# Kernel tuning notes

Measured on AMD Instinct MI355X. Metric: run time of the kernel, lower is better.

## Reference

```python
import jax, jax.numpy as jnp
import numpy as np

T, B, E, H, L = 512, 64, 300, 800, 3  # seq, batch, embed, per-layer hidden, layers


def setup_inputs() -> dict:
    key = jax.random.key(0)
    ks = jax.random.split(key, 8)
    s = 0.05
    return {
        "sent": jax.random.normal(ks[0], (T, B, E), jnp.float32),
        "lengths": jax.random.randint(ks[1], (B,), 1, T + 1),
        "W0": jax.random.normal(ks[2], (E, 3 * H), jnp.float32) * s,
        "b0": jnp.zeros((3 * H,), jnp.float32),
        "W1": jax.random.normal(ks[3], (H, 3 * H), jnp.float32) * s,
        "b1": jnp.zeros((3 * H,), jnp.float32),
        "W2": jax.random.normal(ks[4], (H, 3 * H), jnp.float32) * s,
        "b2": jnp.zeros((3 * H,), jnp.float32),
    }


def _fo_pool(f, z):
    # c_t = f_t * z_t + (1 - f_t) * c_{t-1}, c_0 = 0  (ForgetMult)
    # linear recurrence c_t = a_t * c_{t-1} + b_t with a = 1-f, b = f*z
    a = 1.0 - f
    b = f * z
    def comb(c1, c2):
        a1, b1 = c1
        a2, b2 = c2
        return (a2 * a1, a2 * b1 + b2)
    _, C = jax.lax.associative_scan(comb, (a, b), axis=0)
    return C  # [T,B,H]; initial state is zero so C is exactly the pooled state


def _qrnn_layer(x, W, b):
    g = jnp.einsum('tbe,eh->tbh', x, W) + b  # [T,B,3H]
    z, f, o = jnp.split(g, 3, axis=-1)
    C = _fo_pool(jax.nn.sigmoid(f), jnp.tanh(z))
    return jax.nn.sigmoid(o) * C, C[-1]


def reference(sent, lengths, W0, b0, W1, b1, W2, b2):
    h = sent
    finals = []
    for W, bb in ((W0, b0), (W1, b1), (W2, b2)):
        h, c_last = _qrnn_layer(h, W, bb)
        finals.append(c_last)
    hn = jnp.stack(finals, axis=0)            # [L,B,H]
    out = jnp.transpose(hn, (1, 0, 2)).reshape(B, L * H)  # [B, L*H]
    return out
```

## Files before the change

### kernel.cpp

```cpp
#include <hip/hip_runtime.h>
#include <hip/hip_bf16.h>
#include <cstdint>
#include <cstddef>


typedef __bf16 bf16_t;
typedef __bf16 bf16x8 __attribute__((ext_vector_type(8)));
typedef float f32x4 __attribute__((ext_vector_type(4)));

#define T_C 128
#define NCHUNK 4
#define BATCH 64
#define EMB 300
#define HID 800
#define LDH 832
#define MC (T_C * BATCH)
#define CAST_OPS (MC * 320 / 8)

__device__ __forceinline__ float fast_sigmoid(float x) {
  return 1.0f / (1.0f + __expf(-x));
}
__device__ __forceinline__ float fast_tanh(float x) {
  return 2.0f / (1.0f + __expf(-2.0f * x)) - 1.0f;
}
__device__ __forceinline__ float b2f(uint32_t u) {
  union { uint32_t i; float f; } x;
  x.i = u << 16;
  return x.f;
}

__device__ __forceinline__ void cast_op(const float* __restrict__ X,
                                        bf16_t* __restrict__ Y, int cc,
                                        int id) {
  const int rr = id / 40, cb = id - rr * 40;
  const int b = rr >> 7, t = rr & 127;
  const float* src = X + (size_t)((cc * 128 + t) * 64 + b) * EMB + cb * 8;
  bf16x8 w;
  if (cb < 37) {
    const f32x4 v0 = *(const f32x4*)src;
    const f32x4 v1 = *(const f32x4*)(src + 4);
#pragma unroll
    for (int e = 0; e < 4; ++e) {
      w[e] = (bf16_t)v0[e];
      w[e + 4] = (bf16_t)v1[e];
    }
  } else {
#pragma unroll
    for (int e = 0; e < 8; ++e) {
      const int col = cb * 8 + e;
      float v = (col < EMB) ? src[e] : (col == EMB ? 1.0f : 0.0f);
      w[e] = (bf16_t)v;
    }
  }
  *(bf16x8*)&Y[((size_t)cc * MC + rr) * 320 + cb * 8] = w;
}

__global__ __launch_bounds__(256) void prep_all(
    const float* __restrict__ W0, const float* __restrict__ W1,
    const float* __restrict__ W2, const float* __restrict__ B0,
    const float* __restrict__ B1, const float* __restrict__ B2,
    bf16_t* __restrict__ M0, bf16_t* __restrict__ M1, bf16_t* __restrict__ Z2,
    const float* __restrict__ sent, bf16_t* __restrict__ A0) {
  const int z = blockIdx.z;
  if (z == 3) {
    const int id = (blockIdx.y * gridDim.x + blockIdx.x) * 256 + threadIdx.x;
    if (id < CAST_OPS) cast_op(sent, A0, 0, id);
    return;
  }
  const float* W = z == 0 ? W0 : (z == 1 ? W1 : W2);
  const float* Bv = z == 0 ? B0 : (z == 1 ? B1 : B2);
  bf16_t* Wt = z == 0 ? M0 : (z == 1 ? M1 : Z2);
  const int K = z == 0 ? 300 : 800;
  const int Kpad = z == 0 ? 320 : 832;
  const int Npad = (z < 2) ? 2496 : 1664;
  const int i = blockIdx.x, j = blockIdx.y;
  if (i * 32 >= Npad || j * 32 >= Kpad) return;
  __shared__ float tile[32][33];
  const int tx = threadIdx.x & 31, ty = threadIdx.x >> 5;
#pragma unroll
  for (int r = 0; r < 32; r += 8) {
    const int k = j * 32 + ty + r;
    const int n = i * 32 + tx;
    int h, src;
    if (z < 2) {
      const int jt = n / 192, rr = n - jt * 192;
      if (rr < 128) {
        h = jt * 64 + (rr >> 1);
        src = (rr & 1) * 800 + h;
      } else {
        h = jt * 64 + (rr - 128);
        src = 1600 + h;
      }
    } else {
      h = n >> 1;
      src = (n & 1) * 800 + h;
    }
    float v = 0.0f;
    if (h < 800) {
      if (k < K) v = W[(size_t)k * 2400 + src];
      else if (k == K) v = Bv[src];
    }
    tile[ty + r][tx] = v;
  }
  __syncthreads();
#pragma unroll
  for (int r = 0; r < 32; r += 8) {
    const int n = i * 32 + ty + r, k = j * 32 + tx;
    if (n < Npad && k < Kpad)
      Wt[(size_t)n * Kpad + k] = (bf16_t)tile[tx][ty + r];
  }
}

__device__ __forceinline__ void stage16(const bf16_t* gp, bf16_t* lp) {
  __builtin_amdgcn_global_load_lds((__attribute__((address_space(1))) void*)gp,
                                   (__attribute__((address_space(3))) void*)lp,
                                   16, 0, 0);
}

template <int NTF, int ETS>
__device__ __forceinline__ void gemm_tile_to_lds(
    const bf16_t* __restrict__ A, const bf16_t* __restrict__ Bt,
    bf16_t* __restrict__ S, int K, int mBase, int nBase) {
  bf16_t* As = S;
  bf16_t* Bs = S + 8192;
  const int tid = threadIdx.x;
  const int wave = tid >> 6, lane = tid & 63;
  const int wm = wave >> 1, wn = wave & 1;
  const int srow = tid >> 3;
  const int scolSw = ((tid & 7) ^ (srow & 7)) * 8;
  const size_t aBase = (size_t)(mBase + srow) * K + scolSw;
  const size_t bBase = (size_t)(nBase + srow) * K + scolSw;
  const int ldsOff = tid * 8;

  f32x4 acc[4][NTF];
#pragma unroll
  for (int mt = 0; mt < 4; ++mt)
#pragma unroll
    for (int nt = 0; nt < NTF; ++nt) {
      f32x4 zz = {0.0f, 0.0f, 0.0f, 0.0f};
      acc[mt][nt] = zz;
    }

  const int fr = lane & 15, fq = lane >> 4;
  const int x0 = fr & 7;
  const int ckEl0 = (fq ^ x0) * 8;
  const int ckEl1 = ((4 + fq) ^ x0) * 8;

  for (int k0 = 0; k0 < K; k0 += 64) {
#pragma unroll
    for (int p = 0; p < 4; ++p)
      stage16(A + aBase + (size_t)(32 * p) * K + k0, &As[ldsOff + p * 2048]);
#pragma unroll
    for (int p = 0; p < NTF; ++p)
      stage16(Bt + bBase + (size_t)(32 * p) * K + k0, &Bs[ldsOff + p * 2048]);
    __syncthreads();
#pragma unroll
    for (int kh = 0; kh < 2; ++kh) {
      const int ck = kh ? ckEl1 : ckEl0;
      bf16x8 af[4], bfv[NTF];
#pragma unroll
      for (int mt = 0; mt < 4; ++mt)
        af[mt] = *(const bf16x8*)&As[(wm * 64 + mt * 16 + fr) * 64 + ck];
#pragma unroll
      for (int nt = 0; nt < NTF; ++nt)
        bfv[nt] = *(const bf16x8*)&Bs[(wn * (16 * NTF) + nt * 16 + fr) * 64 + ck];
#pragma unroll
      for (int mt = 0; mt < 4; ++mt)
#pragma unroll
        for (int nt = 0; nt < NTF; ++nt)
          acc[mt][nt] = __builtin_amdgcn_mfma_f32_16x16x32_bf16(
              af[mt], bfv[nt], acc[mt][nt], 0, 0, 0);
    }
    __syncthreads();
  }
  bf16_t* Et = S;
#pragma unroll
  for (int mt = 0; mt < 4; ++mt)
#pragma unroll
    for (int nt = 0; nt < NTF; ++nt)
#pragma unroll
      for (int r = 0; r < 4; ++r)
        Et[(wm * 64 + mt * 16 + fq * 4 + r) * ETS + wn * (16 * NTF) + nt * 16 +
           fr] = (bf16_t)acc[mt][nt][r];
  __syncthreads();
}

__device__ __forceinline__ void scan_h_body(
    const bf16_t* __restrict__ A, const bf16_t* __restrict__ Wm,
    bf16_t* __restrict__ Hout, float* __restrict__ carry,
    float* __restrict__ outC, int K, int outOff, int first, int last, int b,
    int ntile, bf16_t* S, float (*SA)[64], float (*SB)[64], float (*SC)[64]) {
  gemm_tile_to_lds<6, 196>(A, Wm, S, K, b * 128, ntile * 192);

  const uint32_t* Ep = (const uint32_t*)S;
  const int tid = threadIdx.x;
  const int hl = tid & 63, s = tid >> 6;
  const int h = ntile * 64 + hl;
  const bool hOK = (h < HID);

  float av[32], bv[32];
  float Aa = 1.0f, Bb = 0.0f;
#pragma unroll
  for (int q = 0; q < 32; ++q) {
    const int t = s * 32 + q;
    const uint32_t v = Ep[t * 98 + hl];
    const float zv = fast_tanh(b2f(v & 0xffffu));
    const float fv = fast_sigmoid(b2f(v >> 16));
    av[q] = 1.0f - fv;
    bv[q] = fv * zv;
    Aa *= av[q];
    Bb = fmaf(av[q], Bb, bv[q]);
  }
  SA[s][hl] = Aa;
  SB[s][hl] = Bb;
  __syncthreads();
  if (tid < 64) {
    const int h2 = ntile * 64 + tid;
    const bool ok2 = (h2 < HID);
    float c = (first || !ok2) ? 0.0f : carry[b * HID + h2];
#pragma unroll
    for (int ss = 0; ss < 4; ++ss) {
      SC[ss][tid] = c;
      c = fmaf(SA[ss][tid], c, SB[ss][tid]);
    }
    if (ok2) {
      carry[b * HID + h2] = c;
      if (last) outC[b * 2400 + outOff + h2] = c;
    }
  }
  __syncthreads();
  const bf16_t padv = (h == HID) ? (bf16_t)1.0f : (bf16_t)0.0f;
  float c = SC[s][hl];
#pragma unroll
  for (int q = 0; q < 32; ++q) {
    const int t = s * 32 + q;
    c = fmaf(av[q], c, bv[q]);
    const float o = fast_sigmoid((float)S[t * 196 + 128 + hl]);
    Hout[(size_t)(b * 128 + t) * LDH + h] = hOK ? (bf16_t)(o * c) : padv;
  }
}

__device__ __forceinline__ void scan_c_body(
    const bf16_t* __restrict__ A, const bf16_t* __restrict__ Wzf,
    float* __restrict__ carry, float* __restrict__ outC, int K, int outOff,
    int first, int last, int b, int ntile, bf16_t* S, float (*SA)[64],
    float (*SB)[64]) {
  gemm_tile_to_lds<4, 140>(A, Wzf, S, K, b * 128, ntile * 128);

  const uint32_t* Ep = (const uint32_t*)S;
  const int tid = threadIdx.x;
  const int hl = tid & 63, s = tid >> 6;

  float Aa = 1.0f, Bb = 0.0f;
#pragma unroll
  for (int q = 0; q < 32; ++q) {
    const int t = s * 32 + q;
    const uint32_t v = Ep[t * 70 + hl];
    const float zv = fast_tanh(b2f(v & 0xffffu));
    const float fv = fast_sigmoid(b2f(v >> 16));
    const float a = 1.0f - fv;
    Aa *= a;
    Bb = fmaf(a, Bb, fv * zv);
  }
  SA[s][hl] = Aa;
  SB[s][hl] = Bb;
  __syncthreads();
  if (tid < 64) {
    const int h2 = ntile * 64 + tid;
    const bool ok2 = (h2 < HID);
    float c = (first || !ok2) ? 0.0f : carry[b * HID + h2];
#pragma unroll
    for (int ss = 0; ss < 4; ++ss) c = fmaf(SA[ss][tid], c, SB[ss][tid]);
    if (ok2) {
      carry[b * HID + h2] = c;
      if (last) outC[b * 2400 + outOff + h2] = c;
    }
  }
}

__device__ __forceinline__ void block_tile(int& b, int& ntile) {
  const int nT = 13;
  const int L = blockIdx.y * nT + blockIdx.x;
  const int xcd = L & 7, j = L >> 3;
  b = xcd * 8 + j / nT;
  ntile = j % nT;
}

struct Role {
  const bf16_t* A;
  const bf16_t* W;
  bf16_t* Hout;
  float* carry;
  int K;
  int outOff;
  int type;
  int first;
  int last;
};

__global__ __launch_bounds__(256, 3) void gemm_scan_multi(
    Role r0, Role r1, Role r2, Role r3, float* __restrict__ outC) {
  __shared__ __align__(16) bf16_t S[25088];
  __shared__ float SA[4][64], SB[4][64], SC[4][64];
  const Role r = blockIdx.z == 0
                     ? r0
                     : (blockIdx.z == 1 ? r1 : (blockIdx.z == 2 ? r2 : r3));
  if (r.type == 3) {
    int id = (blockIdx.y * gridDim.x + blockIdx.x) * 256 + threadIdx.x;
    const int stride = gridDim.x * gridDim.y * 256;
#pragma unroll
    for (int it = 0; it < 2; ++it, id += stride)
      if (id < CAST_OPS) cast_op((const float*)r.A, r.Hout, r.outOff, id);
    return;
  }
  int b, ntile;
  block_tile(b, ntile);
  if (r.type == 1)
    scan_h_body(r.A, r.W, r.Hout, r.carry, outC, r.K, r.outOff, r.first,
                r.last, b, ntile, S, SA, SB, SC);
  else
    scan_c_body(r.A, r.W, r.carry, outC, r.K, r.outOff, r.first, r.last, b,
                ntile, S, SA, SB);
}

__global__ __launch_bounds__(256, 4) void gemm_scan_c4(
    const bf16_t* __restrict__ A, const bf16_t* __restrict__ Wzf,
    float* __restrict__ carry, float* __restrict__ outC, int K, int outOff,
    int first, int last) {
  __shared__ __align__(16) bf16_t S[17920];
  __shared__ float SA[4][64], SB[4][64];
  int b, ntile;
  block_tile(b, ntile);
  scan_c_body(A, Wzf, carry, outC, K, outOff, first, last, b, ntile, S, SA,
              SB);
}

extern "C" void kernel_launch(void* const* d_in, const int* in_sizes, int n_in,
                              void* d_out, int out_size, void* d_ws, size_t ws_size,
                              hipStream_t stream) {
  const float* sent = (const float*)d_in[0];
  const float* W0 = (const float*)d_in[2];
  const float* b0 = (const float*)d_in[3];
  const float* W1 = (const float*)d_in[4];
  const float* b1 = (const float*)d_in[5];
  const float* W2 = (const float*)d_in[6];
  const float* b2 = (const float*)d_in[7];
  float* out = (float*)d_out;

  char* ws = (char*)d_ws;
  size_t off = 0;
  auto alloc = [&](size_t bytes) {
    void* p = ws + off;
    off += (bytes + 255) & ~(size_t)255;
    return p;
  };
  bf16_t* Wm0 = (bf16_t*)alloc((size_t)2496 * 320 * 2);
  bf16_t* Wm1 = (bf16_t*)alloc((size_t)2496 * 832 * 2);
  bf16_t* Wzf2 = (bf16_t*)alloc((size_t)1664 * 832 * 2);
  bf16_t* A0 = (bf16_t*)alloc((size_t)32768 * 320 * 2);
  bf16_t* H0buf[2], *H1buf[2];
  H0buf[0] = (bf16_t*)alloc((size_t)MC * LDH * 2);
  H0buf[1] = (bf16_t*)alloc((size_t)MC * LDH * 2);
  H1buf[0] = (bf16_t*)alloc((size_t)MC * LDH * 2);
  H1buf[1] = (bf16_t*)alloc((size_t)MC * LDH * 2);
  float* car0 = (float*)alloc((size_t)BATCH * HID * 4);
  float* car1 = (float*)alloc((size_t)BATCH * HID * 4);
  float* car2 = (float*)alloc((size_t)BATCH * HID * 4);
  if (off > ws_size) return;

  prep_all<<<dim3(78, 26, 4), 256, 0, stream>>>(W0, W1, W2, b0, b1, b2, Wm0,
                                                Wm1, Wzf2, sent, A0);

  auto mkL0 = [&](int c) -> Role {
    return Role{A0 + (size_t)c * MC * 320, Wm0, H0buf[c & 1], car0,
                320, 0, 1, c == 0, c == NCHUNK - 1};
  };
  auto mkL1 = [&](int c) -> Role {
    return Role{H0buf[c & 1], Wm1, H1buf[c & 1], car1,
                832, 800, 1, c == 0, c == NCHUNK - 1};
  };
  auto mkL2 = [&](int c) -> Role {
    return Role{H1buf[c & 1], Wzf2, nullptr, car2,
                832, 1600, 2, c == 0, c == NCHUNK - 1};
  };
  auto mkCast = [&](int c) -> Role {
    return Role{(const bf16_t*)sent, nullptr, A0, nullptr, 0, c, 3, 0, 0};
  };

  {
    Role a = mkL0(0), c1 = mkCast(1), c2 = mkCast(2), c3 = mkCast(3);
    gemm_scan_multi<<<dim3(13, 64, 4), 256, 0, stream>>>(a, c1, c2, c3, out);
  }
  {
    Role a = mkL1(0), b_ = mkL0(1);
    gemm_scan_multi<<<dim3(13, 64, 2), 256, 0, stream>>>(a, b_, b_, b_, out);
  }
  for (int c = 1; c <= 2; ++c) {
    Role a = mkL1(c), b_ = mkL2(c - 1), d = mkL0(c + 1);
    gemm_scan_multi<<<dim3(13, 64, 3), 256, 0, stream>>>(a, b_, d, d, out);
  }
  {
    Role a = mkL1(3), b_ = mkL2(2);
    gemm_scan_multi<<<dim3(13, 64, 2), 256, 0, stream>>>(a, b_, b_, b_, out);
  }
  gemm_scan_c4<<<dim3(13, 64), 256, 0, stream>>>(H1buf[1], Wzf2, car2, out,
                                                 832, 1600, 0, 1);
}
```

Before: 461.7 us.

## Scan directly on MFMA accumulator registers instead of staging GEMM output in LDS

Removes the LDS epilogue that wrote the GEMM tile as bf16 and read it back for the forget-mult scan. The scan now runs on the MFMA accumulator registers directly, using 8 time segments per column. For this to work, the weight columns and the time rows of the input are permuted so that z/f/o for the same hidden unit land in matching lanes. The LDS footprint shrinks and a sync disappears, at the cost of more registers per thread and a more involved permutation of rows and weights. Explicit bf16 rounding of a and b is kept so numerics stay close to the previous path.

```diff
diff --git a/kernel.cpp b/kernel.cpp
--- a/kernel.cpp
+++ b/kernel.cpp
@@ -28,13 +28,22 @@
   x.i = u << 16;
   return x.f;
 }
+__device__ __forceinline__ uint32_t f2u16(float v) {
+  union { bf16_t h; uint16_t u; } x;
+  x.h = (bf16_t)v;
+  return (uint32_t)x.u;
+}
+
+__device__ __forceinline__ int rowperm(int i) {
+  return (i & 0xC3) | ((i & 0x30) >> 2) | ((i & 0x0C) << 2);
+}
 
 __device__ __forceinline__ void cast_op(const float* __restrict__ X,
                                         bf16_t* __restrict__ Y, int cc,
                                         int id) {
   const int rr = id / 40, cb = id - rr * 40;
-  const int b = rr >> 7, t = rr & 127;
-  const float* src = X + (size_t)((cc * 128 + t) * 64 + b) * EMB + cb * 8;
+  const int b = rr >> 7, tl = rowperm(rr & 127);
+  const float* src = X + (size_t)((cc * 128 + tl) * 64 + b) * EMB + cb * 8;
   bf16x8 w;
   if (cb < 37) {
     const f32x4 v0 = *(const f32x4*)src;
@@ -83,17 +92,23 @@
     const int n = i * 32 + tx;
     int h, src;
     if (z < 2) {
-      const int jt = n / 192, rr = n - jt * 192;
-      if (rr < 128) {
-        h = jt * 64 + (rr >> 1);
-        src = (rr & 1) * 800 + h;
+      const int jt = n / 192, u0 = n - jt * 192;
+      const int w = u0 / 96, u = u0 - w * 96;
+      if (u < 64) {
+        const int p = u >> 5, g = (u >> 4) & 1, fc = u & 15;
+        h = jt * 64 + w * 32 + p * 16 + fc;
+        src = g * 800 + h;
       } else {
-        h = jt * 64 + (rr - 128);
+        const int q = u - 64;
+        h = jt * 64 + w * 32 + q;
         src = 1600 + h;
       }
     } else {
-      h = n >> 1;
-      src = (n & 1) * 800 + h;
+      const int jt = n >> 7, u0 = n & 127;
+      const int w = u0 >> 6, u = u0 & 63;
+      const int p = u >> 5, g = (u >> 4) & 1, fc = u & 15;
+      h = jt * 64 + w * 32 + p * 16 + fc;
+      src = g * 800 + h;
     }
     float v = 0.0f;
     if (h < 800) {
@@ -117,10 +132,11 @@
                                    16, 0, 0);
 }
 
-template <int NTF, int ETS>
-__device__ __forceinline__ void gemm_tile_to_lds(
+template <int NTF>
+__device__ __forceinline__ void gemm_tile_regs(
     const bf16_t* __restrict__ A, const bf16_t* __restrict__ Bt,
-    bf16_t* __restrict__ S, int K, int mBase, int nBase) {
+    bf16_t* __restrict__ S, int K, int mBase, int nBase,
+    f32x4 (&acc)[4][NTF]) {
   bf16_t* As = S;
   bf16_t* Bs = S + 8192;
   const int tid = threadIdx.x;
@@ -132,7 +148,6 @@
   const size_t bBase = (size_t)(nBase + srow) * K + scolSw;
   const int ldsOff = tid * 8;
 
-  f32x4 acc[4][NTF];
 #pragma unroll
   for (int mt = 0; mt < 4; ++mt)
 #pragma unroll
@@ -173,16 +188,6 @@
     }
     __syncthreads();
   }
-  bf16_t* Et = S;
-#pragma unroll
-  for (int mt = 0; mt < 4; ++mt)
-#pragma unroll
-    for (int nt = 0; nt < NTF; ++nt)
-#pragma unroll
-      for (int r = 0; r < 4; ++r)
-        Et[(wm * 64 + mt * 16 + fq * 4 + r) * ETS + wn * (16 * NTF) + nt * 16 +
-           fr] = (bf16_t)acc[mt][nt][r];
-  __syncthreads();
 }
 
 __device__ __forceinline__ void scan_h_body(
@@ -190,36 +195,43 @@
     bf16_t* __restrict__ Hout, float* __restrict__ carry,
     float* __restrict__ outC, int K, int outOff, int first, int last, int b,
     int ntile, bf16_t* S, float (*SA)[64], float (*SB)[64], float (*SC)[64]) {
-  gemm_tile_to_lds<6, 196>(A, Wm, S, K, b * 128, ntile * 192);
-
-  const uint32_t* Ep = (const uint32_t*)S;
+  f32x4 acc[4][6];
+  gemm_tile_regs<6>(A, Wm, S, K, b * 128, ntile * 192, acc);
+
   const int tid = threadIdx.x;
-  const int hl = tid & 63, s = tid >> 6;
-  const int h = ntile * 64 + hl;
-  const bool hOK = (h < HID);
-
-  float av[32], bv[32];
-  float Aa = 1.0f, Bb = 0.0f;
-#pragma unroll
-  for (int q = 0; q < 32; ++q) {
-    const int t = s * 32 + q;
-    const uint32_t v = Ep[t * 98 + hl];
-    const float zv = fast_tanh(b2f(v & 0xffffu));
-    const float fv = fast_sigmoid(b2f(v >> 16));
-    av[q] = 1.0f - fv;
-    bv[q] = fv * zv;
-    Aa *= av[q];
-    Bb = fmaf(av[q], Bb, bv[q]);
-  }
-  SA[s][hl] = Aa;
-  SB[s][hl] = Bb;
+  const int wave = tid >> 6, lane = tid & 63;
+  const int wm = wave >> 1, wn = wave & 1;
+  const int fr = lane & 15, fq = lane >> 4;
+  const int seg = wm * 4 + fq;
+
+  uint32_t ab[2][16];
+#pragma unroll
+  for (int p = 0; p < 2; ++p) {
+    float Aa = 1.0f, Bb = 0.0f;
+#pragma unroll
+    for (int mt = 0; mt < 4; ++mt)
+#pragma unroll
+      for (int r = 0; r < 4; ++r) {
+        const int q = mt * 4 + r;
+        const float zv = fast_tanh(acc[mt][2 * p][r]);
+        const float fv = fast_sigmoid(acc[mt][2 * p + 1][r]);
+        const uint32_t ua = f2u16(1.0f - fv), ub = f2u16(fv * zv);
+        ab[p][q] = ua | (ub << 16);
+        const float af = b2f(ua), bf_ = b2f(ub << 16 >> 16);
+        Aa *= af;
+        Bb = fmaf(af, Bb, b2f(ub));
+      }
+    const int cl = wn * 32 + p * 16 + fr;
+    SA[seg][cl] = Aa;
+    SB[seg][cl] = Bb;
+  }
   __syncthreads();
   if (tid < 64) {
     const int h2 = ntile * 64 + tid;
     const bool ok2 = (h2 < HID);
     float c = (first || !ok2) ? 0.0f : carry[b * HID + h2];
 #pragma unroll
-    for (int ss = 0; ss < 4; ++ss) {
+    for (int ss = 0; ss < 8; ++ss) {
       SC[ss][tid] = c;
       c = fmaf(SA[ss][tid], c, SB[ss][tid]);
     }
@@ -229,14 +241,23 @@
     }
   }
   __syncthreads();
-  const bf16_t padv = (h == HID) ? (bf16_t)1.0f : (bf16_t)0.0f;
-  float c = SC[s][hl];
-#pragma unroll
-  for (int q = 0; q < 32; ++q) {
-    const int t = s * 32 + q;
-    c = fmaf(av[q], c, bv[q]);
-    const float o = fast_sigmoid((float)S[t * 196 + 128 + hl]);
-    Hout[(size_t)(b * 128 + t) * LDH + h] = hOK ? (bf16_t)(o * c) : padv;
+#pragma unroll
+  for (int p = 0; p < 2; ++p) {
+    const int cl = wn * 32 + p * 16 + fr;
+    const int h = ntile * 64 + cl;
+    const bool hOK = (h < HID);
+    const bf16_t padv = (h == HID) ? (bf16_t)1.0f : (bf16_t)0.0f;
+    float c = SC[seg][cl];
+#pragma unroll
+    for (int mt = 0; mt < 4; ++mt)
+#pragma unroll
+      for (int r = 0; r < 4; ++r) {
+        const int q = mt * 4 + r;
+        c = fmaf(b2f(ab[p][q] & 0xffffu), c, b2f(ab[p][q] >> 16));
+        const float o = fast_sigmoid(acc[mt][4 + p][r]);
+        const int row = b * 128 + wm * 64 + mt * 16 + fq * 4 + r;
+        Hout[(size_t)row * LDH + h] = hOK ? (bf16_t)(o * c) : padv;
+      }
   }
 }
 
@@ -245,32 +266,40 @@
     float* __restrict__ carry, float* __restrict__ outC, int K, int outOff,
     int first, int last, int b, int ntile, bf16_t* S, float (*SA)[64],
     float (*SB)[64]) {
-  gemm_tile_to_lds<4, 140>(A, Wzf, S, K, b * 128, ntile * 128);
-
-  const uint32_t* Ep = (const uint32_t*)S;
+  f32x4 acc[4][4];
+  gemm_tile_regs<4>(A, Wzf, S, K, b * 128, ntile * 128, acc);
+
   const int tid = threadIdx.x;
-  const int hl = tid & 63, s = tid >> 6;
-
-  float Aa = 1.0f, Bb = 0.0f;
-#pragma unroll
-  for (int q = 0; q < 32; ++q) {
-    const int t = s * 32 + q;
-    const uint32_t v = Ep[t * 70 + hl];
-    const float zv = fast_tanh(b2f(v & 0xffffu));
-    const float fv = fast_sigmoid(b2f(v >> 16));
-    const float a = 1.0f - fv;
-    Aa *= a;
-    Bb = fmaf(a, Bb, fv * zv);
-  }
-  SA[s][hl] = Aa;
-  SB[s][hl] = Bb;
+  const int wave = tid >> 6, lane = tid & 63;
+  const int wm = wave >> 1, wn = wave & 1;
+  const int fr = lane & 15, fq = lane >> 4;
+  const int seg = wm * 4 + fq;
+
+#pragma unroll
+  for (int p = 0; p < 2; ++p) {
+    float Aa = 1.0f, Bb = 0.0f;
+#pragma unroll
+    for (int mt = 0; mt < 4; ++mt)
+#pragma unroll
+      for (int r = 0; r < 4; ++r) {
+        const float zv = fast_tanh(acc[mt][2 * p][r]);
+        const float fv = fast_sigmoid(acc[mt][2 * p + 1][r]);
+        const float af = b2f(f2u16(1.0f - fv));
+        const float bf_ = b2f(f2u16(fv * zv));
+        Aa *= af;
+        Bb = fmaf(af, Bb, bf_);
+      }
+    const int cl = wn * 32 + p * 16 + fr;
+    SA[seg][cl] = Aa;
+    SB[seg][cl] = Bb;
+  }
   __syncthreads();
   if (tid < 64) {
     const int h2 = ntile * 64 + tid;
     const bool ok2 = (h2 < HID);
     float c = (first || !ok2) ? 0.0f : carry[b * HID + h2];
 #pragma unroll
-    for (int ss = 0; ss < 4; ++ss) c = fmaf(SA[ss][tid], c, SB[ss][tid]);
+    for (int ss = 0; ss < 8; ++ss) c = fmaf(SA[ss][tid], c, SB[ss][tid]);
     if (ok2) {
       carry[b * HID + h2] = c;
       if (last) outC[b * 2400 + outOff + h2] = c;
@@ -300,8 +329,8 @@
 
 __global__ __launch_bounds__(256, 3) void gemm_scan_multi(
     Role r0, Role r1, Role r2, Role r3, float* __restrict__ outC) {
-  __shared__ __align__(16) bf16_t S[25088];
-  __shared__ float SA[4][64], SB[4][64], SC[4][64];
+  __shared__ __align__(16) bf16_t S[20480];
+  __shared__ float SA[8][64], SB[8][64], SC[8][64];
   const Role r = blockIdx.z == 0
                      ? r0
                      : (blockIdx.z == 1 ? r1 : (blockIdx.z == 2 ? r2 : r3));
@@ -327,8 +356,8 @@
     const bf16_t* __restrict__ A, const bf16_t* __restrict__ Wzf,
     float* __restrict__ carry, float* __restrict__ outC, int K, int outOff,
     int first, int last) {
-  __shared__ __align__(16) bf16_t S[17920];
-  __shared__ float SA[4][64], SB[4][64];
+  __shared__ __align__(16) bf16_t S[16384];
+  __shared__ float SA[8][64], SB[8][64];
   int b, ntile;
   block_tile(b, ntile);
   scan_c_body(A, Wzf, carry, outC, K, outOff, first, last, b, ntile, S, SA,
```

Measured after the change: 476.4 us. 1.03x slower.
